# Kernel tuning notes

Hardware: AMD Instinct MI355X
Metric: run time of the kernel (lower is better)

## Reference

```python
import jax, jax.numpy as jnp
import numpy as np


def setup_inputs() -> dict:
    key = jax.random.key(0)
    T, B, D, H = 512, 64, 512, 512
    k0, k1, k2, k3 = jax.random.split(key, 4)
    x = jax.random.normal(k0, (T, B, D), dtype=jnp.float32)
    # packed-sequence lengths, descending (as PackedSequence requires), at least T//2
    lengths = jnp.sort(jax.random.randint(k1, (B,), T // 2, T + 1))[::-1].astype(jnp.int64)
    s = 1.0 / np.sqrt(H)
    # gates stacked in order (i, f, c, o): same math as 8 separate per-gate linears
    Wx = jax.random.normal(k2, (4 * H, D), dtype=jnp.float32) * s
    Wh = jax.random.normal(k3, (4 * H, H), dtype=jnp.float32) * s
    # reset_parameters(): b_i = b_c = b_o = 0, b_f = 1
    b = jnp.concatenate([jnp.zeros(H), jnp.ones(H), jnp.zeros(2 * H)]).astype(jnp.float32)
    return {"x": x, "lengths": lengths, "Wx": Wx, "Wh": Wh, "b": b}


def reference(x, lengths, Wx, Wh, b):
    T, B, D = x.shape
    H = Wh.shape[1]
    # input projections for all timesteps at once (one big GEMM)
    xg = jnp.einsum('tbd,gd->tbg', x, Wx) + b  # [T, B, 4H]
    # validity mask per (t, b): packed recurrence only updates active rows
    mask = (jnp.arange(T)[:, None] < lengths[None, :])[..., None]  # [T, B, 1]

    def step(carry, inp):
        h, c = carry
        xg_t, m = inp
        g = xg_t + h @ Wh.T  # [B, 4H]
        i, f, cc, o = jnp.split(g, 4, axis=-1)
        i = jax.nn.sigmoid(i)
        f = jax.nn.sigmoid(f)
        o = jax.nn.sigmoid(o)
        c_t = f * c + i * jnp.tanh(cc)
        h_t = o * jnp.tanh(c_t)
        c_new = jnp.where(m, c_t, c)
        h_new = jnp.where(m, h_t, h)
        out_t = jnp.where(m, h_new, jnp.zeros((), x.dtype))
        return (h_new, c_new), out_t

    h0 = jnp.zeros((B, H), dtype=x.dtype)
    (h_T, c_T), out = jax.lax.scan(step, (h0, h0), (xg, mask))
    return out  # padded equivalent of the PackedSequence output, [T, B, H]
```

## Files before the change

### kernel.cpp

```cpp
#include <hip/hip_runtime.h>
#include <stdint.h>


#define TT 512
#define BB 64
#define DD 512
#define HH 512
#define NWG 256
#define NTHR 512
#define GR 8

typedef short short8 __attribute__((ext_vector_type(8)));
typedef float f32x4 __attribute__((ext_vector_type(4)));

__device__ __forceinline__ uint16_t bf16_rne(float f) {
  uint32_t u = __float_as_uint(f);
  u += 0x7fffu + ((u >> 16) & 1u);
  return (uint16_t)(u >> 16);
}

__device__ __forceinline__ void split2(float f, uint16_t &hi, uint16_t &lo) {
  uint16_t h = bf16_rne(f);
  hi = h;
  lo = bf16_rne(f - __uint_as_float(((uint32_t)h) << 16));
}

__device__ __forceinline__ float sigf(float v) { return 1.0f / (1.0f + __expf(-v)); }
__device__ __forceinline__ float tanh_(float v) {
  return 1.0f - 2.0f / (__expf(2.0f * v) + 1.0f);
}

__global__ void build_frags(const float* __restrict__ W, uint32_t* __restrict__ frag) {
  const int tid = blockIdx.x * 256 + threadIdx.x;
  const int lane = tid & 63;
  const int ks = (tid >> 6) & 15;
  const int nblk = tid >> 10;
  const int col = nblk * 16 + (lane & 15);
  const int k0 = ks * 32 + ((lane >> 4) << 3);
  const float* src = W + (size_t)col * 512 + k0;
  float4 a = *(const float4*)(src);
  float4 b = *(const float4*)(src + 4);
  float v[8] = {a.x, a.y, a.z, a.w, b.x, b.y, b.z, b.w};
  uint32_t hw[4], lw[4];
#pragma unroll
  for (int j = 0; j < 4; ++j) {
    uint16_t h0, l0, h1, l1;
    split2(v[2 * j], h0, l0);
    split2(v[2 * j + 1], h1, l1);
    hw[j] = (uint32_t)h0 | ((uint32_t)h1 << 16);
    lw[j] = (uint32_t)l0 | ((uint32_t)l1 << 16);
  }
  uint4* dst = (uint4*)(frag + (size_t)tid * 8);
  dst[0] = make_uint4(hw[0], hw[1], hw[2], hw[3]);
  dst[1] = make_uint4(lw[0], lw[1], lw[2], lw[3]);
}

__global__ __launch_bounds__(NTHR, 2) void lstm6(
    const float* __restrict__ x, const int* __restrict__ len,
    const float* __restrict__ bias, const uint32_t* __restrict__ fragWx,
    const uint32_t* __restrict__ fragWh, uint32_t* __restrict__ h_pair,
    float* __restrict__ out) {
  const int tid = threadIdx.x;
  const int lane = tid & 63;
  const int wave = tid >> 6;
  const int gp = wave >> 1;
  const int kh = wave & 1;
  const int group = blockIdx.x & 7;
  const int jblk = blockIdx.x >> 3;
  const int b0 = group * GR;
  const int j0 = jblk << 4;
  uint32_t* hbase = h_pair + (size_t)group * 2 * (GR * HH);

  __shared__ uint16_t HAH[2][GR * 512];
  __shared__ uint16_t HAL[2][GR * 512];
  __shared__ uint16_t XH[GR * 512];
  __shared__ uint16_t XL[GR * 512];
  __shared__ float ex[8][GR][16];
  __shared__ float c_st[GR][16];
  __shared__ float h_st[GR][16];
  __shared__ float bias_l[4][16];
  __shared__ int len_l[GR];

  if (tid < GR * 16) {
    c_st[tid >> 4][tid & 15] = 0.0f;
    h_st[tid >> 4][tid & 15] = 0.0f;
  }
  if (tid < 64) bias_l[tid >> 4][tid & 15] = bias[(size_t)(tid >> 4) * HH + j0 + (tid & 15)];
  if (tid < GR) len_l[tid] = len[b0 + tid];

  short8 bxh[8], bxl[8], bhh[8], bhl[8];
  {
    const int nblk = gp * 32 + jblk;
#pragma unroll
    for (int ksl = 0; ksl < 8; ++ksl) {
      const size_t idx = ((size_t)(nblk * 16 + kh * 8 + ksl) * 64 + lane) * 8;
      bxh[ksl] = __builtin_bit_cast(short8, *(const uint4*)(fragWx + idx));
      bxl[ksl] = __builtin_bit_cast(short8, *(const uint4*)(fragWx + idx + 4));
      bhh[ksl] = __builtin_bit_cast(short8, *(const uint4*)(fragWh + idx));
      bhl[ksl] = __builtin_bit_cast(short8, *(const uint4*)(fragWh + idx + 4));
    }
  }

  const int arow = lane & 7;
  const int achk = (lane >> 4) << 4;
  const int axr = arow << 4;
  const char* xrowH = (const char*)XH + arow * 1024;
  const char* xrowL = (const char*)XL + arow * 1024;

  f32x4 hh = {0.f, 0.f, 0.f, 0.f}, lh = {0.f, 0.f, 0.f, 0.f}, hl = {0.f, 0.f, 0.f, 0.f};
  float4 xp[2];

  const uint64_t MK2 = 0x4000400040004000ull;
  const uint32_t CM = ~0x40004000u;

#define LOAD_XP(tt)                                                            \
  _Pragma("unroll") for (int i = 0; i < 2; ++i) {                              \
    const int flat4 = i * 2048 + tid * 4;                                      \
    const int row = flat4 >> 9;                                                \
    const int col = flat4 & 511;                                               \
    xp[i] = *(const float4*)(x + ((size_t)(tt) * BB + b0 + row) * DD + col);   \
  }

#define STAGE_XP()                                                             \
  _Pragma("unroll") for (int i = 0; i < 2; ++i) {                              \
    const int flat4 = i * 2048 + tid * 4;                                      \
    const int row = flat4 >> 9;                                                \
    const int col = flat4 & 511;                                               \
    uint16_t h0, l0, h1, l1, h2, l2, h3, l3;                                   \
    split2(xp[i].x, h0, l0);                                                   \
    split2(xp[i].y, h1, l1);                                                   \
    split2(xp[i].z, h2, l2);                                                   \
    split2(xp[i].w, h3, l3);                                                   \
    const uint32_t hw0 = (uint32_t)h0 | ((uint32_t)h1 << 16);                  \
    const uint32_t hw1 = (uint32_t)h2 | ((uint32_t)h3 << 16);                  \
    const uint32_t lw0 = (uint32_t)l0 | ((uint32_t)l1 << 16);                  \
    const uint32_t lw1 = (uint32_t)l2 | ((uint32_t)l3 << 16);                  \
    const int off = row * 1024 + ((col * 2) ^ (row << 4));                     \
    *(uint2*)((char*)XH + off) = make_uint2(hw0, hw1);                         \
    *(uint2*)((char*)XL + off) = make_uint2(lw0, lw1);                         \
  }

#define X_MFMA()                                                               \
  hh = (f32x4){0.f, 0.f, 0.f, 0.f};                                           \
  lh = (f32x4){0.f, 0.f, 0.f, 0.f};                                           \
  hl = (f32x4){0.f, 0.f, 0.f, 0.f};                                           \
  _Pragma("unroll") for (int ksl = 0; ksl < 8; ++ksl) {                        \
    const int off = ((kh * 8 + ksl) * 64 + achk) ^ axr;                        \
    short8 ah = *(const short8*)(xrowH + off);                                 \
    short8 al = *(const short8*)(xrowL + off);                                 \
    hh = __builtin_amdgcn_mfma_f32_16x16x32_bf16(ah, bxh[ksl], hh, 0, 0, 0);   \
    lh = __builtin_amdgcn_mfma_f32_16x16x32_bf16(al, bxh[ksl], lh, 0, 0, 0);   \
    hl = __builtin_amdgcn_mfma_f32_16x16x32_bf16(ah, bxl[ksl], hl, 0, 0, 0);   \
  }

  LOAD_XP(0);
  __syncthreads();
  STAGE_XP();
  __syncthreads();
  X_MFMA();
  LOAD_XP(1);

  for (int t = 0; t < TT; ++t) {
    const int rbuf = t & 1;
    const int wbuf = rbuf ^ 1;

    if (t > 0) {
      const uint32_t tg = (((uint32_t)(t - 1)) >> 1) & 3u;
      const uint32_t Ed = ((tg & 1u) << 14) | ((tg >> 1) << 30);
      const uint64_t EX2 = ((uint64_t)Ed << 32) | Ed;
      const unsigned long long* pb =
          (const unsigned long long*)(hbase + (size_t)rbuf * (GR * HH)) +
          (size_t)tid * 4;
      uint64_t w0, w1, w2, w3;
      for (;;) {
        w0 = __hip_atomic_load(pb + 0, __ATOMIC_RELAXED, __HIP_MEMORY_SCOPE_AGENT);
        w1 = __hip_atomic_load(pb + 1, __ATOMIC_RELAXED, __HIP_MEMORY_SCOPE_AGENT);
        w2 = __hip_atomic_load(pb + 2, __ATOMIC_RELAXED, __HIP_MEMORY_SCOPE_AGENT);
        w3 = __hip_atomic_load(pb + 3, __ATOMIC_RELAXED, __HIP_MEMORY_SCOPE_AGENT);
        const uint64_t bad =
            (((w0 ^ EX2) | (w1 ^ EX2) | (w2 ^ EX2) | (w3 ^ EX2)) & MK2);
        if (bad == 0ull) break;
      }

      {
        uint32_t d0 = (uint32_t)w0 & CM, d1 = (uint32_t)(w0 >> 32) & CM;
        uint32_t d2 = (uint32_t)w1 & CM, d3 = (uint32_t)(w1 >> 32) & CM;
        uint32_t d4 = (uint32_t)w2 & CM, d5 = (uint32_t)(w2 >> 32) & CM;
        uint32_t d6 = (uint32_t)w3 & CM, d7 = (uint32_t)(w3 >> 32) & CM;
        const uint32_t hi0 = (d0 & 0xFFFFu) | (d1 << 16);
        const uint32_t lo0 = (d0 >> 16) | (d1 & 0xFFFF0000u);
        const uint32_t hi1 = (d2 & 0xFFFFu) | (d3 << 16);
        const uint32_t lo1 = (d2 >> 16) | (d3 & 0xFFFF0000u);
        const uint32_t hi2 = (d4 & 0xFFFFu) | (d5 << 16);
        const uint32_t lo2 = (d4 >> 16) | (d5 & 0xFFFF0000u);
        const uint32_t hi3 = (d6 & 0xFFFFu) | (d7 << 16);
        const uint32_t lo3 = (d6 >> 16) | (d7 & 0xFFFF0000u);
        const int woff = wave * 1024 + ((lane * 16) ^ (wave << 4));
        *(uint4*)((char*)HAH[rbuf] + woff) = make_uint4(hi0, hi1, hi2, hi3);
        *(uint4*)((char*)HAL[rbuf] + woff) = make_uint4(lo0, lo1, lo2, lo3);
      }
      __syncthreads();

      {
        const char* rowH = (const char*)HAH[rbuf] + arow * 1024;
        const char* rowL = (const char*)HAL[rbuf] + arow * 1024;
#pragma unroll
        for (int ksl = 0; ksl < 8; ++ksl) {
          const int off = ((kh * 8 + ksl) * 64 + achk) ^ axr;
          short8 ah = *(const short8*)(rowH + off);
          short8 al = *(const short8*)(rowL + off);
          hh = __builtin_amdgcn_mfma_f32_16x16x32_bf16(ah, bhh[ksl], hh, 0, 0, 0);
          lh = __builtin_amdgcn_mfma_f32_16x16x32_bf16(al, bhh[ksl], lh, 0, 0, 0);
          hl = __builtin_amdgcn_mfma_f32_16x16x32_bf16(ah, bhl[ksl], hl, 0, 0, 0);
        }
      }
    }

    {
      const int crow = (lane >> 4) << 2;
      const int ccol = lane & 15;
      if (crow < GR) {
#pragma unroll
        for (int r = 0; r < 4; ++r) ex[wave][crow + r][ccol] = hh[r] + lh[r] + hl[r];
      }
    }
    __syncthreads();

    if (tid < GR * 16) {
      const int brow = tid >> 4;
      const int jc = tid & 15;
      const float p0 = ex[0][brow][jc] + ex[1][brow][jc] + bias_l[0][jc];
      const float p1 = ex[2][brow][jc] + ex[3][brow][jc] + bias_l[1][jc];
      const float p2 = ex[4][brow][jc] + ex[5][brow][jc] + bias_l[2][jc];
      const float p3 = ex[6][brow][jc] + ex[7][brow][jc] + bias_l[3][jc];
      const float ig = sigf(p0);
      const float fg = sigf(p1);
      const float cc = tanh_(p2);
      const float og = sigf(p3);
      const float co = c_st[brow][jc];
      const float ct = fg * co + ig * cc;
      const float ht = og * tanh_(ct);
      const bool m = (t < len_l[brow]);
      const float cn = m ? ct : co;
      const float hn = m ? ht : h_st[brow][jc];
      uint16_t ph, pl;
      split2(hn, ph, pl);
      const uint32_t tagw = (((uint32_t)t) >> 1) & 3u;
      const uint32_t TB = ((tagw & 1u) << 14) | ((tagw >> 1) << 30);
      __hip_atomic_store(hbase + (size_t)wbuf * (GR * HH) + brow * HH + j0 + jc,
                         ((uint32_t)ph | ((uint32_t)pl << 16)) | TB,
                         __ATOMIC_RELAXED, __HIP_MEMORY_SCOPE_AGENT);
      out[((size_t)t * BB + b0 + brow) * HH + j0 + jc] = m ? ht : 0.0f;
      c_st[brow][jc] = cn;
      h_st[brow][jc] = hn;
    }

    if (t + 1 < TT) {
      STAGE_XP();
      __syncthreads();
      X_MFMA();
      LOAD_XP(min(t + 2, TT - 1));
    }
  }
#undef LOAD_XP
#undef STAGE_XP
#undef X_MFMA
}

extern "C" void kernel_launch(void* const* d_in, const int* in_sizes, int n_in,
                              void* d_out, int out_size, void* d_ws, size_t ws_size,
                              hipStream_t stream) {
  const float* x = (const float*)d_in[0];
  const int* len = (const int*)d_in[1];
  const float* Wx = (const float*)d_in[2];
  const float* Wh = (const float*)d_in[3];
  const float* bias = (const float*)d_in[4];
  float* out = (float*)d_out;

  const size_t FRAG_DW = (size_t)128 * 16 * 64 * 8;
  const size_t HP_DW = (size_t)8 * 2 * GR * HH;
  uint32_t* fragWx = (uint32_t*)d_ws;
  uint32_t* fragWh = fragWx + FRAG_DW;
  uint32_t* h_pair = fragWh + FRAG_DW;

  hipMemsetAsync(h_pair, 0xFF, HP_DW * 4, stream);

  build_frags<<<dim3(512), dim3(256), 0, stream>>>(Wx, fragWx);
  build_frags<<<dim3(512), dim3(256), 0, stream>>>(Wh, fragWh);

  void* args[] = {(void*)&x,      (void*)&len,    (void*)&bias, (void*)&fragWx,
                  (void*)&fragWh, (void*)&h_pair, (void*)&out};
  hipLaunchCooperativeKernel((void*)lstm6, dim3(NWG), dim3(NTHR), args, 0, stream);
}
```

Baseline: 1.436 ms.

## Replace per-step block barriers with half-block LDS counters and double-buffer X staging

```diff
diff --git a/kernel.cpp b/kernel.cpp
--- a/kernel.cpp
+++ b/kernel.cpp
@@ -55,7 +55,7 @@
   dst[1] = make_uint4(lw[0], lw[1], lw[2], lw[3]);
 }
 
-__global__ __launch_bounds__(NTHR, 2) void lstm6(
+__global__ __launch_bounds__(NTHR, 2) void lstm7(
     const float* __restrict__ x, const int* __restrict__ len,
     const float* __restrict__ bias, const uint32_t* __restrict__ fragWx,
     const uint32_t* __restrict__ fragWh, uint32_t* __restrict__ h_pair,
@@ -73,14 +73,16 @@
 
   __shared__ uint16_t HAH[2][GR * 512];
   __shared__ uint16_t HAL[2][GR * 512];
-  __shared__ uint16_t XH[GR * 512];
-  __shared__ uint16_t XL[GR * 512];
+  __shared__ uint16_t XH[2][GR * 512];
+  __shared__ uint16_t XL[2][GR * 512];
   __shared__ float ex[8][GR][16];
   __shared__ float c_st[GR][16];
   __shared__ float h_st[GR][16];
   __shared__ float bias_l[4][16];
   __shared__ int len_l[GR];
-
+  __shared__ uint32_t hcnt[2];
+
+  if (tid < 2) hcnt[tid] = 0u;
   if (tid < GR * 16) {
     c_st[tid >> 4][tid & 15] = 0.0f;
     h_st[tid >> 4][tid & 15] = 0.0f;
@@ -104,8 +106,10 @@
   const int arow = lane & 7;
   const int achk = (lane >> 4) << 4;
   const int axr = arow << 4;
-  const char* xrowH = (const char*)XH + arow * 1024;
-  const char* xrowL = (const char*)XL + arow * 1024;
+
+  const int q = ((wave >> 1) << 6) | lane;
+  const int prow = q >> 5;
+  const int pch = q & 31;
 
   f32x4 hh = {0.f, 0.f, 0.f, 0.f}, lh = {0.f, 0.f, 0.f, 0.f}, hl = {0.f, 0.f, 0.f, 0.f};
   float4 xp[2];
@@ -121,7 +125,7 @@
     xp[i] = *(const float4*)(x + ((size_t)(tt) * BB + b0 + row) * DD + col);   \
   }
 
-#define STAGE_XP()                                                             \
+#define STAGE_XP(PB)                                                           \
   _Pragma("unroll") for (int i = 0; i < 2; ++i) {                              \
     const int flat4 = i * 2048 + tid * 4;                                      \
     const int row = flat4 >> 9;                                                \
@@ -136,29 +140,37 @@
     const uint32_t lw0 = (uint32_t)l0 | ((uint32_t)l1 << 16);                  \
     const uint32_t lw1 = (uint32_t)l2 | ((uint32_t)l3 << 16);                  \
     const int off = row * 1024 + ((col * 2) ^ (row << 4));                     \
-    *(uint2*)((char*)XH + off) = make_uint2(hw0, hw1);                         \
-    *(uint2*)((char*)XL + off) = make_uint2(lw0, lw1);                         \
-  }
-
-#define X_MFMA()                                                               \
+    *(uint2*)((char*)XH[PB] + off) = make_uint2(hw0, hw1);                     \
+    *(uint2*)((char*)XL[PB] + off) = make_uint2(lw0, lw1);                     \
+  }
+
+#define X_MFMA(PB)                                                             \
   hh = (f32x4){0.f, 0.f, 0.f, 0.f};                                           \
   lh = (f32x4){0.f, 0.f, 0.f, 0.f};                                           \
   hl = (f32x4){0.f, 0.f, 0.f, 0.f};                                           \
-  _Pragma("unroll") for (int ksl = 0; ksl < 8; ++ksl) {                        \
-    const int off = ((kh * 8 + ksl) * 64 + achk) ^ axr;                        \
-    short8 ah = *(const short8*)(xrowH + off);                                 \
-    short8 al = *(const short8*)(xrowL + off);                                 \
-    hh = __builtin_amdgcn_mfma_f32_16x16x32_bf16(ah, bxh[ksl], hh, 0, 0, 0);   \
-    lh = __builtin_amdgcn_mfma_f32_16x16x32_bf16(al, bxh[ksl], lh, 0, 0, 0);   \
-    hl = __builtin_amdgcn_mfma_f32_16x16x32_bf16(ah, bxl[ksl], hl, 0, 0, 0);   \
+  {                                                                            \
+    const char* rH = (const char*)XH[PB] + arow * 1024;                        \
+    const char* rL = (const char*)XL[PB] + arow * 1024;                        \
+    _Pragma("unroll") for (int ksl = 0; ksl < 8; ++ksl) {                      \
+      const int off = ((kh * 8 + ksl) * 64 + achk) ^ axr;                      \
+      short8 ah = *(const short8*)(rH + off);                                  \
+      short8 al = *(const short8*)(rL + off);                                  \
+      hh = __builtin_amdgcn_mfma_f32_16x16x32_bf16(ah, bxh[ksl], hh, 0, 0, 0); \
+      lh = __builtin_amdgcn_mfma_f32_16x16x32_bf16(al, bxh[ksl], lh, 0, 0, 0); \
+      hl = __builtin_amdgcn_mfma_f32_16x16x32_bf16(ah, bxl[ksl], hl, 0, 0, 0); \
+    }                                                                          \
   }
 
   LOAD_XP(0);
   __syncthreads();
-  STAGE_XP();
+  STAGE_XP(0);
   __syncthreads();
-  X_MFMA();
+  X_MFMA(0);
   LOAD_XP(1);
+  STAGE_XP(1);
+  LOAD_XP(2);
+
+  uint32_t htg = 0;
 
   for (int t = 0; t < TT; ++t) {
     const int rbuf = t & 1;
@@ -170,7 +182,7 @@
       const uint64_t EX2 = ((uint64_t)Ed << 32) | Ed;
       const unsigned long long* pb =
           (const unsigned long long*)(hbase + (size_t)rbuf * (GR * HH)) +
-          (size_t)tid * 4;
+          prow * 256 + pch * 4 + (kh ? 128 : 0);
       uint64_t w0, w1, w2, w3;
       for (;;) {
         w0 = __hip_atomic_load(pb + 0, __ATOMIC_RELAXED, __HIP_MEMORY_SCOPE_AGENT);
@@ -195,11 +207,19 @@
         const uint32_t lo2 = (d4 >> 16) | (d5 & 0xFFFF0000u);
         const uint32_t hi3 = (d6 & 0xFFFFu) | (d7 << 16);
         const uint32_t lo3 = (d6 >> 16) | (d7 & 0xFFFF0000u);
-        const int woff = wave * 1024 + ((lane * 16) ^ (wave << 4));
+        const int woff = prow * 1024 + ((pch * 16 + kh * 512) ^ (prow << 4));
         *(uint4*)((char*)HAH[rbuf] + woff) = make_uint4(hi0, hi1, hi2, hi3);
         *(uint4*)((char*)HAL[rbuf] + woff) = make_uint4(lo0, lo1, lo2, lo3);
       }
-      __syncthreads();
+
+      htg += 4;
+      if (lane == 0)
+        __hip_atomic_fetch_add(&hcnt[kh], 1u, __ATOMIC_ACQ_REL,
+                               __HIP_MEMORY_SCOPE_WORKGROUP);
+      while (__hip_atomic_load(&hcnt[kh], __ATOMIC_ACQUIRE,
+                               __HIP_MEMORY_SCOPE_WORKGROUP) < htg) {
+      }
+      asm volatile("" ::: "memory");
 
       {
         const char* rowH = (const char*)HAH[rbuf] + arow * 1024;
@@ -256,10 +276,9 @@
     }
 
     if (t + 1 < TT) {
-      STAGE_XP();
-      __syncthreads();
-      X_MFMA();
-      LOAD_XP(min(t + 2, TT - 1));
+      STAGE_XP(rbuf);
+      X_MFMA(wbuf);
+      LOAD_XP(min(t + 3, TT - 1));
     }
   }
 #undef LOAD_XP
@@ -290,5 +309,5 @@
 
   void* args[] = {(void*)&x,      (void*)&len,    (void*)&bias, (void*)&fragWx,
                   (void*)&fragWh, (void*)&h_pair, (void*)&out};
-  hipLaunchCooperativeKernel((void*)lstm6, dim3(NWG), dim3(NTHR), args, 0, stream);
-}
+  hipLaunchCooperativeKernel((void*)lstm7, dim3(NWG), dim3(NTHR), args, 0, stream);
+}
```

Measured after the change: 1.175 ms, median of 2. 18.2% less time.
